# Optimization experiments

Measured on AMD Instinct MI355X. Metric: run time of the kernel, lower is better.

The kernel has to match this reference:

```python
import jax, jax.numpy as jnp
import numpy as np
import math

B, S, H, NH, DK, K = 256, 200, 768, 12, 64, 64
EPS = 1e-12

def setup_inputs() -> dict:
    key = jax.random.key(0)
    ks = jax.random.split(key, 8)
    sc = 0.02
    return {
        "x": jax.random.normal(ks[0], (B, S, H), dtype=jnp.float32),
        "mask": jnp.ones((B, 1, S), dtype=jnp.float32),
        "Wq": jax.random.normal(ks[1], (H, H), dtype=jnp.float32) * sc,
        "bq": jnp.zeros((H,), dtype=jnp.float32),
        "Wk": jax.random.normal(ks[2], (H, H), dtype=jnp.float32) * sc,
        "bk": jnp.zeros((H,), dtype=jnp.float32),
        "Wv": jax.random.normal(ks[3], (H, H), dtype=jnp.float32) * sc,
        "bv": jnp.zeros((H,), dtype=jnp.float32),
        "We": jax.random.normal(ks[4], (K, S), dtype=jnp.float32) * sc,
        "be": jnp.zeros((K,), dtype=jnp.float32),
        "Wf": jax.random.normal(ks[5], (K, S), dtype=jnp.float32) * sc,
        "bf": jnp.zeros((K,), dtype=jnp.float32),
        "Wd": jax.random.normal(ks[6], (H, H), dtype=jnp.float32) * sc,
        "bd": jnp.zeros((H,), dtype=jnp.float32),
        "gamma": jnp.ones((H,), dtype=jnp.float32),
        "beta": jnp.zeros((H,), dtype=jnp.float32),
    }

def _heads(t):  # [B,S,H] -> [B,NH,S,DK]
    return t.reshape(B, S, NH, DK).transpose(0, 2, 1, 3)

def reference(x, mask, Wq, bq, Wk, bk, Wv, bv, We, be, Wf, bf, Wd, bd, gamma, beta):
    q = _heads(x @ Wq.T + bq)
    k = _heads(x @ Wk.T + bk)
    v = _heads(x @ Wv.T + bv)
    m = mask[:, 0:1, :, None]            # [B,1,S,1]
    k = k * m
    v = v * m
    # Linformer seq projections: E on value, F on key (applied along seq axis)
    v = jnp.einsum("bhsd,ks->bhkd", v, We) + be[:, None]   # [B,NH,K,DK]
    k = jnp.einsum("bhsd,ks->bhkd", k, Wf) + bf[:, None]   # [B,NH,K,DK]
    scores = jnp.einsum("bhqd,bhkd->bhqk", q, k) / math.sqrt(DK)
    p_attn = jax.nn.softmax(scores, axis=-1)               # [B,NH,S,K]
    ctx = jnp.einsum("bhqk,bhkd->bhqd", p_attn, v)         # [B,NH,S,DK]
    ctx = ctx.transpose(0, 2, 1, 3).reshape(B, S, H)
    h = ctx @ Wd.T + bd + x                                # dense + residual (dropout=0)
    mu = jnp.mean(h, axis=-1, keepdims=True)
    var = jnp.mean(jnp.square(h - mu), axis=-1, keepdims=True)
    out = (h - mu) / jnp.sqrt(var + EPS) * gamma + beta
    return out, p_attn
```

## Files before the change

### kernel.cpp

```cpp
#include <hip/hip_runtime.h>
#include <stdint.h>

typedef unsigned short u16;
typedef short bf16x8 __attribute__((ext_vector_type(8)));
typedef float f32x4 __attribute__((ext_vector_type(4)));
typedef unsigned short u16x4 __attribute__((ext_vector_type(4)));

#define NB   256
#define NS   200
#define NHID 768
#define NHEAD 12
#define NDK  64
#define NK   64
#define NBH  (NB*NHEAD)
#define NM   (NB*NS)
#define SP   224

__device__ __forceinline__ u16 f2b(float f){
  unsigned u = __builtin_bit_cast(unsigned, f);
  return (u16)((u + 0x7FFFu + ((u>>16)&1u)) >> 16);
}
__device__ __forceinline__ float b2f(u16 b){
  return __builtin_bit_cast(float, (unsigned)b << 16);
}
__device__ __forceinline__ f32x4 mfma16(bf16x8 a, bf16x8 b, f32x4 c){
  return __builtin_amdgcn_mfma_f32_16x16x32_bf16(a, b, c, 0, 0, 0);
}
__device__ __forceinline__ void gload16(u16* l, const u16* g){
  __builtin_amdgcn_global_load_lds(
      (const __attribute__((address_space(1))) void*)g,
      (__attribute__((address_space(3))) void*)l, 16, 0, 0);
}

__global__ __launch_bounds__(256) void prep_kernel(
    const float* __restrict__ Wq, const float* __restrict__ Wk,
    const float* __restrict__ Wv, const float* __restrict__ Wd,
    const float* __restrict__ Wf, const float* __restrict__ We,
    const float* __restrict__ mask,
    u16* __restrict__ Wqb, u16* __restrict__ Wkb,
    u16* __restrict__ Wvb, u16* __restrict__ Wdb,
    u16* __restrict__ Wfeb, float* __restrict__ rs)
{
  const int blk = blockIdx.x, t = threadIdx.x;
  const int i = blk*256 + t;
  Wqb[i]=f2b(Wq[i]); Wkb[i]=f2b(Wk[i]); Wvb[i]=f2b(Wv[i]); Wdb[i]=f2b(Wd[i]);
  if (blk < 128 && t < SP){
    float v = 0.f;
    if (t < NS) v = (blk<64) ? Wf[blk*NS+t] : We[(blk-64)*NS+t];
    Wfeb[blk*SP+t] = f2b(v);
  }
  if (blk >= 1024 && blk < 1280 && t < 128){
    const int b = blk-1024;
    const float* src = (t<64) ? (Wf + t*NS) : (We + (t-64)*NS);
    float acc = 0.f;
    for (int s=0;s<NS;s++) acc += src[s]*mask[b*NS+s];
    rs[b*128+t] = acc;
  }
}

__global__ __launch_bounds__(256) void transpose_x(
    const float* __restrict__ x, const float* __restrict__ mask,
    u16* __restrict__ xb, u16* __restrict__ xbT)
{
  __shared__ u16 LT[64*232];
  const int t = threadIdx.x, b = blockIdx.x, n0 = blockIdx.y*64;
  for (int i=0;i<50;i++){
    const int idx = i*256 + t;
    const int s = idx>>6, n = idx&63;
    const size_t gi = ((size_t)b*NS + s)*NHID + n0 + n;
    const float v = x[gi];
    xb[gi] = f2b(v);
    const float mv = mask[b*NS+s];
    LT[n*232 + s] = f2b(v*mv);
  }
  __syncthreads();
  const int row = t>>2, cb = t&3;
  u16* dst = xbT + (size_t)b*NHID*SP + (size_t)(n0+row)*SP;
  for (int i=0;i<7;i++){
    const int c = cb + i*4;
    bf16x8 vv = (c<25) ? *(const bf16x8*)&LT[row*232 + c*8] : (bf16x8)0;
    *(bf16x8*)&dst[c*8] = vv;
  }
}

__global__ __launch_bounds__(256) void gemm_yfe(
    const u16* __restrict__ Wfeb, const u16* __restrict__ xbT, u16* __restrict__ yfe)
{
  __shared__ u16 Al[128*64];
  __shared__ u16 Bl[128*64];
  const int t=threadIdx.x, w=t>>6, lane=t&63, hi=lane>>4, lo=lane&15;
  const int sr=lane>>3, sc=lane&7;
  const int b=blockIdx.x, col0=blockIdx.y*128;
  const u16* Bg = xbT + (size_t)b*NHID*SP;
  f32x4 acc[4][4];
#pragma unroll
  for(int i=0;i<4;i++)
#pragma unroll
    for(int j=0;j<4;j++) acc[i][j]=(f32x4)0.0f;
  const u16* Ab=&Al[((w>>1)*64+lo)*64 + hi*8];
  const u16* Bb=&Bl[((w&1)*64+lo)*64 + hi*8];

  for (int kt=0; kt<192; kt+=64){
#pragma unroll
    for (int i8=0;i8<4;i8++){
      const int r = w*32 + i8*8 + sr;
      gload16(&Al[r*64 + sc*8], Wfeb + (size_t)r*SP + kt + sc*8);
      gload16(&Bl[r*64 + sc*8], Bg + (size_t)(col0+r)*SP + kt + sc*8);
    }
    asm volatile("s_waitcnt vmcnt(0)" ::: "memory");
    __syncthreads();
#pragma unroll
    for (int ks=0; ks<2; ks++){
      bf16x8 a[4], bfr[4];
#pragma unroll
      for (int i=0;i<4;i++) a[i]   = *(const bf16x8*)(Ab + i*16*64 + ks*32);
#pragma unroll
      for (int j=0;j<4;j++) bfr[j] = *(const bf16x8*)(Bb + j*16*64 + ks*32);
#pragma unroll
      for (int i=0;i<4;i++)
#pragma unroll
        for (int j=0;j<4;j++) acc[i][j] = mfma16(a[i], bfr[j], acc[i][j]);
    }
    __syncthreads();
  }
#pragma unroll
  for (int i8=0;i8<2;i8++){
    const int r2 = w*32 + i8*16 + (lane>>2);
    gload16(&Al[r2*32 + (lane&3)*8], Wfeb + (size_t)r2*SP + 192 + (lane&3)*8);
    gload16(&Bl[r2*32 + (lane&3)*8], Bg + (size_t)(col0+r2)*SP + 192 + (lane&3)*8);
  }
  asm volatile("s_waitcnt vmcnt(0)" ::: "memory");
  __syncthreads();
  {
    bf16x8 a[4], bfr[4];
#pragma unroll
    for (int i=0;i<4;i++) a[i]   = *(const bf16x8*)&Al[((w>>1)*64+i*16+lo)*32 + hi*8];
#pragma unroll
    for (int j=0;j<4;j++) bfr[j] = *(const bf16x8*)&Bl[((w&1)*64+j*16+lo)*32 + hi*8];
#pragma unroll
    for (int i=0;i<4;i++)
#pragma unroll
      for (int j=0;j<4;j++) acc[i][j] = mfma16(a[i], bfr[j], acc[i][j]);
  }
  const int mbase=(w>>1)*64, nbase=col0+(w&1)*64;
#pragma unroll
  for (int i=0;i<4;i++)
#pragma unroll
    for (int r=0;r<4;r++){
      const int m = mbase + i*16 + hi*4 + r;
#pragma unroll
      for (int j=0;j<4;j++){
        const int n = nbase + j*16 + lo;
        yfe[(size_t)b*98304 + (size_t)m*NHID + n] = f2b(acc[i][j][r]);
      }
    }
}

template<int EPI>
__global__ __launch_bounds__(512, 2) void gemm_ring(
    const u16* __restrict__ Ag_, const u16* __restrict__ Bg_,
    const float* __restrict__ bias, const u16* __restrict__ resid,
    u16* __restrict__ Cout)
{
  __shared__ u16 AS[4][8192];
  __shared__ u16 BS[4][8192];
  const int t = threadIdx.x;
  const int w = t>>6, lane = t&63, hi = lane>>4, lo = lane&15;
  const int wm = w>>2, wn = w&3;
  const int bid = blockIdx.x;
  const int row0 = ((bid/24)*8 + (bid&7))*256;
  const int col0 = ((bid>>3)%3)*256;
  const u16* Ag = Ag_ + (size_t)row0*NHID;
  const u16* Bg = Bg_ + (size_t)col0*NHID;
  const int rp0 = t>>3, cc = t&7;

  f32x4 acc[8][4];
#pragma unroll
  for (int i=0;i<8;i++)
#pragma unroll
    for (int j=0;j<4;j++) acc[i][j] = (f32x4)0.0f;

  int aoff[8], boff[4];
#pragma unroll
  for (int i=0;i<8;i++){
    const int r = wm*128 + i*16 + lo;
    const int rp = r>>1, c = (r&1)*4 + hi;
    aoff[i] = rp*64 + ((c ^ (rp&7))<<3);
  }
#pragma unroll
  for (int j=0;j<4;j++){
    const int n = wn*64 + j*16 + lo;
    const int rp = n>>1, c = (n&1)*4 + hi;
    boff[j] = rp*64 + ((c ^ (rp&7))<<3);
  }

  auto stage = [&](int s, int kt){
#pragma unroll
    for (int i8=0;i8<2;i8++){
      const int rp = i8*64 + rp0;
      const int c  = cc ^ (rp&7);
      const int grow = rp*2 + (c>>2);
      const int gcol = (c&3)<<3;
      gload16(&AS[s][rp*64 + cc*8], Ag + (size_t)grow*NHID + kt + gcol);
      gload16(&BS[s][rp*64 + cc*8], Bg + (size_t)grow*NHID + kt + gcol);
    }
  };
  auto body = [&](const u16* as_, const u16* bs_){
    bf16x8 av[8], bvv[4];
#pragma unroll
    for (int j=0;j<4;j++) bvv[j] = *(const bf16x8*)(bs_ + boff[j]);
#pragma unroll
    for (int i=0;i<8;i++) av[i] = *(const bf16x8*)(as_ + aoff[i]);
    __builtin_amdgcn_s_setprio(1);
#pragma unroll
    for (int i=0;i<8;i++)
#pragma unroll
      for (int j=0;j<4;j++) acc[i][j] = mfma16(av[i], bvv[j], acc[i][j]);
    __builtin_amdgcn_s_setprio(0);
  };
  auto step = [&](int tt, int s){
    if (tt+3 < 24) stage((s+3)&3, (tt+3)*32);
    body(AS[s], BS[s]);
    if (tt <= 20)      { asm volatile("s_waitcnt vmcnt(8)" ::: "memory"); }
    else if (tt == 21) { asm volatile("s_waitcnt vmcnt(4)" ::: "memory"); }
    else if (tt == 22) { asm volatile("s_waitcnt vmcnt(0)" ::: "memory"); }
    if (tt < 23){
      __builtin_amdgcn_sched_barrier(0);
      asm volatile("s_barrier" ::: "memory");
      __builtin_amdgcn_sched_barrier(0);
    }
  };

  stage(0,0); stage(1,32); stage(2,64);
  asm volatile("s_waitcnt vmcnt(8)" ::: "memory");
  asm volatile("s_barrier" ::: "memory");
  __builtin_amdgcn_sched_barrier(0);

#pragma unroll
  for (int tt=0; tt<24; tt+=4){
    step(tt,0); step(tt+1,1); step(tt+2,2); step(tt+3,3);
  }

#pragma unroll
  for (int i=0;i<8;i++)
#pragma unroll
    for (int q=0;q<4;q++){
      const int m = row0 + wm*128 + i*16 + hi*4 + q;
#pragma unroll
      for (int j=0;j<4;j++){
        const int n = col0 + wn*64 + j*16 + lo;
        float v = acc[i][j][q] + bias[n];
        if constexpr (EPI==0){
          const int b = m/NS, s = m - b*NS;
          Cout[(((size_t)b*NHEAD + (n>>6))*NS + s)*NDK + (n&63)] = f2b(v);
        } else {
          const size_t gi = (size_t)m*NHID + n;
          Cout[gi] = f2b(v + b2f(resid[gi]));
        }
      }
    }
}

__global__ __launch_bounds__(256) void gemm_projkv(
    const u16* __restrict__ yfe, const u16* __restrict__ Wkb,
    const u16* __restrict__ Wvb, const float* __restrict__ rs,
    const float* __restrict__ bk, const float* __restrict__ bv,
    const float* __restrict__ bff, const float* __restrict__ bee,
    u16* __restrict__ kproj, u16* __restrict__ vout)
{
  __shared__ u16 S[192*64];
  const int t=threadIdx.x, w=t>>6, lane=t&63, hi=lane>>4, lo=lane&15;
  const int sr=lane>>3, sc=lane&7;
  const int bid=blockIdx.x;
  const int b = (bid/96)*8 + (bid&7);
  const int jj = (bid>>3)%12;
  const int colb = jj%6, z = jj/6;

  if (z==0){
    u16* Al = S;
    u16* Bl = S + 64*64;
    const int col0=colb*128;
    const u16* yf = yfe + (size_t)b*98304;
    f32x4 acc[2][4];
#pragma unroll
    for(int i=0;i<2;i++)
#pragma unroll
      for(int j=0;j<4;j++) acc[i][j]=(f32x4)0.0f;
    const u16* Ab=&Al[((w>>1)*32+lo)*64 + hi*8];
    const u16* Bb=&Bl[((w&1)*64+lo)*64 + hi*8];
    for (int kt=0; kt<NHID; kt+=64){
#pragma unroll
      for (int i8=0;i8<2;i8++){
        const int r = w*16 + i8*8 + sr;
        gload16(&Al[r*64 + sc*8], yf + (size_t)r*NHID + kt + sc*8);
      }
#pragma unroll
      for (int i8=0;i8<4;i8++){
        const int r = w*32 + i8*8 + sr;
        gload16(&Bl[r*64 + sc*8], Wkb + (size_t)(col0+r)*NHID + kt + sc*8);
      }
      asm volatile("s_waitcnt vmcnt(0)" ::: "memory");
      __syncthreads();
#pragma unroll
      for (int ks=0; ks<2; ks++){
        bf16x8 a[2], bfr[4];
#pragma unroll
        for (int i=0;i<2;i++) a[i]   = *(const bf16x8*)(Ab + i*16*64 + ks*32);
#pragma unroll
        for (int j=0;j<4;j++) bfr[j] = *(const bf16x8*)(Bb + j*16*64 + ks*32);
#pragma unroll
        for (int i=0;i<2;i++)
#pragma unroll
          for (int j=0;j<4;j++) acc[i][j] = mfma16(a[i], bfr[j], acc[i][j]);
      }
      __syncthreads();
    }
    const int mbase=(w>>1)*32, nbase=col0+(w&1)*64;
#pragma unroll
    for (int i=0;i<2;i++)
#pragma unroll
      for (int r=0;r<4;r++){
        const int m = mbase + i*16 + hi*4 + r;
        const float rsv = rs[b*128 + m], bfv = bff[m];
#pragma unroll
        for (int j=0;j<4;j++){
          const int n = nbase + j*16 + lo;
          kproj[(size_t)b*49152 + (size_t)m*NHID + n] = f2b(acc[i][j][r] + rsv*bk[n] + bfv);
        }
      }
  } else {
    u16* Al = S;
    u16* Bl = S + 128*64;
    const int row0=colb*128;
    const u16* ye = yfe + (size_t)b*98304 + 49152;
    f32x4 acc[4][2];
#pragma unroll
    for(int i=0;i<4;i++)
#pragma unroll
      for(int j=0;j<2;j++) acc[i][j]=(f32x4)0.0f;
    const u16* Ab=&Al[((w>>1)*64+lo)*64 + hi*8];
    const u16* Bb=&Bl[((w&1)*32+lo)*64 + hi*8];
    for (int kt=0; kt<NHID; kt+=64){
#pragma unroll
      for (int i8=0;i8<4;i8++){
        const int r = w*32 + i8*8 + sr;
        gload16(&Al[r*64 + sc*8], Wvb + (size_t)(row0+r)*NHID + kt + sc*8);
      }
#pragma unroll
      for (int i8=0;i8<2;i8++){
        const int r = w*16 + i8*8 + sr;
        gload16(&Bl[r*64 + sc*8], ye + (size_t)r*NHID + kt + sc*8);
      }
      asm volatile("s_waitcnt vmcnt(0)" ::: "memory");
      __syncthreads();
#pragma unroll
      for (int ks=0; ks<2; ks++){
        bf16x8 a[4], bfr[2];
#pragma unroll
        for (int i=0;i<4;i++) a[i]   = *(const bf16x8*)(Ab + i*16*64 + ks*32);
#pragma unroll
        for (int j=0;j<2;j++) bfr[j] = *(const bf16x8*)(Bb + j*16*64 + ks*32);
#pragma unroll
        for (int i=0;i<4;i++)
#pragma unroll
          for (int j=0;j<2;j++) acc[i][j] = mfma16(a[i], bfr[j], acc[i][j]);
      }
      __syncthreads();
    }
    const int mbase=row0+(w>>1)*64, nbase=(w&1)*32;
#pragma unroll
    for (int i=0;i<4;i++)
#pragma unroll
      for (int r=0;r<4;r++){
        const int m = mbase + i*16 + hi*4 + r;
        const float bvv = bv[m];
#pragma unroll
        for (int j=0;j<2;j++){
          const int n = nbase + j*16 + lo;
          vout[(size_t)b*49152 + (size_t)m*64 + n] = f2b(acc[i][j][r] + rs[b*128+64+n]*bvv + bee[n]);
        }
      }
  }
}

__global__ __launch_bounds__(256) void attn_kernel(
    const u16* __restrict__ qb,
    const u16* __restrict__ kproj,
    const u16* __restrict__ vprojT,
    float* __restrict__ pout,
    u16* __restrict__ ctxb)
{
  __shared__ u16 QL[208*72];
  __shared__ u16 KP[64*72];
  __shared__ u16 VP[64*72];
  const int t=threadIdx.x, w=t>>6, lane=t&63, hi=lane>>4, lo=lane&15;
  const int bh = blockIdx.x, b=bh/NHEAD, hh=bh%NHEAD;
  for (int c=t;c<1600;c+=256){
    const int row=c>>3, col8=(c&7)*8;
    *(bf16x8*)&QL[row*72+col8] = *(const bf16x8*)(qb + (size_t)bh*12800 + c*8);
  }
  if (t<72){ const int row=200+t/9, col8=(t%9)*8; *(bf16x8*)&QL[row*72+col8]=(bf16x8)0; }
  for (int c=t;c<512;c+=256){
    const int row=c>>3, col8=(c&7)*8;
    *(bf16x8*)&KP[row*72+col8] = *(const bf16x8*)(kproj  + (size_t)b*49152 + (size_t)row*NHID + hh*64 + col8);
    *(bf16x8*)&VP[row*72+col8] = *(const bf16x8*)(vprojT + (size_t)b*49152 + (size_t)(hh*64+row)*64 + col8);
  }
  __syncthreads();
  const int mf0 = (w==0)?0:(1+w*3);
  const int nmf = (w==0)?4:3;
  f32x4 acc[4][4];
#pragma unroll
  for(int i=0;i<4;i++)
#pragma unroll
    for(int j=0;j<4;j++) acc[i][j]=(f32x4)0.0f;
#pragma unroll
  for (int ks=0; ks<2; ks++){
    bf16x8 a[4], bb[4];
#pragma unroll
    for (int j=0;j<4;j++) bb[j]=*(const bf16x8*)&KP[(j*16+lo)*72 + ks*32 + hi*8];
#pragma unroll
    for (int i=0;i<4;i++) if (i<nmf) a[i]=*(const bf16x8*)&QL[((mf0+i)*16+lo)*72 + ks*32 + hi*8];
#pragma unroll
    for (int i=0;i<4;i++) if (i<nmf)
#pragma unroll
      for (int j=0;j<4;j++)
        acc[i][j]=mfma16(a[i],bb[j],acc[i][j]);
  }
  __syncthreads();

#pragma unroll
  for (int i=0;i<4;i++) if (i<nmf){
#pragma unroll
    for (int r=0;r<4;r++){
      const int q = (mf0+i)*16 + hi*4 + r;
      float s0=acc[i][0][r]*0.125f, s1=acc[i][1][r]*0.125f,
            s2=acc[i][2][r]*0.125f, s3=acc[i][3][r]*0.125f;
      float mx=fmaxf(fmaxf(s0,s1),fmaxf(s2,s3));
      mx=fmaxf(mx,__shfl_xor(mx,1)); mx=fmaxf(mx,__shfl_xor(mx,2));
      mx=fmaxf(mx,__shfl_xor(mx,4)); mx=fmaxf(mx,__shfl_xor(mx,8));
      float e0=__expf(s0-mx), e1=__expf(s1-mx), e2=__expf(s2-mx), e3=__expf(s3-mx);
      float sm=e0+e1+e2+e3;
      sm+=__shfl_xor(sm,1); sm+=__shfl_xor(sm,2); sm+=__shfl_xor(sm,4); sm+=__shfl_xor(sm,8);
      const float inv=1.0f/sm;
      const float p0=e0*inv,p1=e1*inv,p2=e2*inv,p3=e3*inv;
      if (q<NS){
        float* pg = pout + ((size_t)bh*NS + q)*NK + lo;
        pg[0]=p0; pg[16]=p1; pg[32]=p2; pg[48]=p3;
      }
      u16* pl = &QL[q*72 + lo];
      pl[0]=f2b(p0); pl[16]=f2b(p1); pl[32]=f2b(p2); pl[48]=f2b(p3);
    }
  }
  f32x4 acc2[4][4];
#pragma unroll
  for(int i=0;i<4;i++)
#pragma unroll
    for(int j=0;j<4;j++) acc2[i][j]=(f32x4)0.0f;
#pragma unroll
  for (int ks=0; ks<2; ks++){
    bf16x8 a[4], bb[4];
#pragma unroll
    for (int j=0;j<4;j++) bb[j]=*(const bf16x8*)&VP[(j*16+lo)*72 + ks*32 + hi*8];
#pragma unroll
    for (int i=0;i<4;i++) if (i<nmf) a[i]=*(const bf16x8*)&QL[((mf0+i)*16+lo)*72 + ks*32 + hi*8];
#pragma unroll
    for (int i=0;i<4;i++) if (i<nmf)
#pragma unroll
      for (int j=0;j<4;j++)
        acc2[i][j]=mfma16(a[i],bb[j],acc2[i][j]);
  }
#pragma unroll
  for (int i=0;i<4;i++) if (i<nmf)
#pragma unroll
    for (int r=0;r<4;r++){
      const int q=(mf0+i)*16+hi*4+r;
      if (q<NS){
#pragma unroll
        for (int j=0;j<4;j++){
          const int d=j*16+lo;
          ctxb[((size_t)b*NS+q)*NHID + hh*NDK + d] = f2b(acc2[i][j][r]);
        }
      }
    }
}

__global__ __launch_bounds__(256) void ln2_kernel(
    const u16* __restrict__ h, const float* __restrict__ gamma,
    const float* __restrict__ beta, float* __restrict__ outp)
{
  const int t = threadIdx.x, wid = t>>6, lane = t&63;
  float g_[12], be_[12];
#pragma unroll
  for (int k=0;k<3;k++){
    float4 gg = *(const float4*)(gamma + lane*12 + k*4);
    float4 bb = *(const float4*)(beta  + lane*12 + k*4);
    g_[k*4+0]=gg.x; g_[k*4+1]=gg.y; g_[k*4+2]=gg.z; g_[k*4+3]=gg.w;
    be_[k*4+0]=bb.x; be_[k*4+1]=bb.y; be_[k*4+2]=bb.z; be_[k*4+3]=bb.w;
  }
  for (int row = blockIdx.x*4 + wid; row < NM; row += 1600*4){
    const u16* hr = h + (size_t)row*NHID + lane*12;
    u16x4 a0 = *(const u16x4*)hr;
    u16x4 a1 = *(const u16x4*)(hr+4);
    u16x4 a2 = *(const u16x4*)(hr+8);
    float v[12];
#pragma unroll
    for (int k=0;k<4;k++){
      v[k]   = b2f(a0[k]);
      v[4+k] = b2f(a1[k]);
      v[8+k] = b2f(a2[k]);
    }
    float s=0.f, q=0.f;
#pragma unroll
    for (int k=0;k<12;k++){ s+=v[k]; q+=v[k]*v[k]; }
#pragma unroll
    for (int m=1;m<64;m<<=1){ s+=__shfl_xor(s,m); q+=__shfl_xor(q,m); }
    const float mu = s*(1.0f/768.0f);
    const float rsv = rsqrtf(q*(1.0f/768.0f) - mu*mu + 1e-12f);
    float* orow = outp + (size_t)row*NHID + lane*12;
#pragma unroll
    for (int k=0;k<12;k++) orow[k] = (v[k]-mu)*rsv*g_[k] + be_[k];
  }
}

extern "C" void kernel_launch(void* const* d_in, const int* in_sizes, int n_in,
                              void* d_out, int out_size, void* d_ws, size_t ws_size,
                              hipStream_t stream)
{
  (void)in_sizes; (void)n_in; (void)out_size; (void)ws_size;
  const float* x    = (const float*)d_in[0];
  const float* mask = (const float*)d_in[1];
  const float* Wq   = (const float*)d_in[2];
  const float* bq   = (const float*)d_in[3];
  const float* Wk   = (const float*)d_in[4];
  const float* bk   = (const float*)d_in[5];
  const float* Wv   = (const float*)d_in[6];
  const float* bv   = (const float*)d_in[7];
  const float* We   = (const float*)d_in[8];
  const float* be   = (const float*)d_in[9];
  const float* Wf   = (const float*)d_in[10];
  const float* bf   = (const float*)d_in[11];
  const float* Wd   = (const float*)d_in[12];
  const float* bd   = (const float*)d_in[13];
  const float* gamma= (const float*)d_in[14];
  const float* beta = (const float*)d_in[15];

  float* out  = (float*)d_out;
  float* pout = out + (size_t)NM*NHID;

  char* ws = (char*)d_ws;
  u16* xb    = (u16*)(ws);
  u16* xbT   = (u16*)(ws + 78643200ull);
  u16* qb    = (u16*)(ws + 78643200ull);
  u16* yfe   = (u16*)(ws + 166723584ull);
  u16* kproj = (u16*)(ws + 217055232ull);
  u16* Wqb   = (u16*)(ws + 242221056ull);
  u16* Wkb   = (u16*)(ws + 243400704ull);
  u16* Wvb   = (u16*)(ws + 244580352ull);
  u16* Wdb   = (u16*)(ws + 245760000ull);
  u16* Wfeb  = (u16*)(ws + 246939648ull);
  float* rsb = (float*)(ws + 246996992ull);
  u16* vprojT= (u16*)(ws + 247128064ull);
  u16* ctxb  = (u16*)(ws + 272293888ull);
  u16* hb    = (u16*)(ws + 350937088ull);

  prep_kernel<<<2304,256,0,stream>>>(Wq,Wk,Wv,Wd,Wf,We,mask,Wqb,Wkb,Wvb,Wdb,Wfeb,rsb);
  transpose_x<<<dim3(NB,12),256,0,stream>>>(x,mask,xb,xbT);
  gemm_yfe<<<dim3(NB,6),256,0,stream>>>(Wfeb,xbT,yfe);
  gemm_ring<0><<<600,512,0,stream>>>(xb,Wqb,bq,nullptr,qb);
  gemm_projkv<<<3072,256,0,stream>>>(yfe,Wkb,Wvb,rsb,bk,bv,bf,be,kproj,vprojT);
  attn_kernel<<<NBH,256,0,stream>>>(qb,kproj,vprojT,pout,ctxb);
  gemm_ring<1><<<600,512,0,stream>>>(ctxb,Wdb,bd,xb,hb);
  ln2_kernel<<<1600,256,0,stream>>>(hb,gamma,beta,out);
}
```

Measured before the change: 553.0 us.

## Pipeline projkv GEMM with 4-stage swizzled LDS ring and nontemporal output stores

Replaces the single-buffered 64-wide K loop in gemm_projkv with a 4-stage, 32-wide K ring buffer. Global loads are issued three tiles ahead, with partial vmcnt waits and one barrier per step, so memory latency overlaps the MFMA work. The LDS layout is XOR-swizzled to reduce bank conflicts, and s_setprio raises priority around the MFMA bursts. Separately, the p_attn stores and the layernorm output stores become nontemporal, and the layernorm stores are vectorised, to reduce cache pollution from streaming writes.

```diff
diff --git a/kernel.cpp b/kernel.cpp
--- a/kernel.cpp
+++ b/kernel.cpp
@@ -268,54 +268,87 @@
     const float* __restrict__ bff, const float* __restrict__ bee,
     u16* __restrict__ kproj, u16* __restrict__ vout)
 {
-  __shared__ u16 S[192*64];
+  __shared__ u16 S[4][192*32];
   const int t=threadIdx.x, w=t>>6, lane=t&63, hi=lane>>4, lo=lane&15;
-  const int sr=lane>>3, sc=lane&7;
   const int bid=blockIdx.x;
   const int b = (bid/96)*8 + (bid&7);
   const int jj = (bid>>3)%12;
   const int colb = jj%6, z = jj/6;
+  const int cc = t&7, rpt = t>>3;
+
+  const u16* yf  = yfe + (size_t)b*98304;
+  const u16* ye  = yfe + (size_t)b*98304 + 49152;
+  const u16* Wk0 = Wkb + (size_t)(colb*128)*NHID;
+  const u16* Wv0 = Wvb + (size_t)(colb*128)*NHID;
+
+  const u16* srcb[3]; int dsto[3];
+#pragma unroll
+  for (int i8=0;i8<3;i8++){
+    const int rp = i8*32 + rpt;
+    const int c  = cc ^ (rp&7);
+    const int grow = rp*2 + (c>>2);
+    const int gcol = (c&3)<<3;
+    dsto[i8] = rp*64 + cc*8;
+    const u16* rb;
+    if (z==0) rb = (grow<64)  ? (yf  + (size_t)grow*NHID)        : (Wk0 + (size_t)(grow-64)*NHID);
+    else      rb = (grow<128) ? (Wv0 + (size_t)grow*NHID)        : (ye  + (size_t)(grow-128)*NHID);
+    srcb[i8] = rb + gcol;
+  }
+  auto off = [&](int r){
+    const int rp = r>>1, c = (r&1)*4 + hi;
+    return rp*64 + ((c ^ (rp&7))<<3);
+  };
+  auto stage = [&](int s, int kt){
+#pragma unroll
+    for (int i8=0;i8<3;i8++) gload16(&S[s][dsto[i8]], srcb[i8] + kt);
+  };
 
   if (z==0){
-    u16* Al = S;
-    u16* Bl = S + 64*64;
-    const int col0=colb*128;
-    const u16* yf = yfe + (size_t)b*98304;
+    int aoff[2], boff[4];
+#pragma unroll
+    for (int i=0;i<2;i++) aoff[i] = off((w>>1)*32 + i*16 + lo);
+#pragma unroll
+    for (int j=0;j<4;j++) boff[j] = off(64 + (w&1)*64 + j*16 + lo);
     f32x4 acc[2][4];
 #pragma unroll
     for(int i=0;i<2;i++)
 #pragma unroll
       for(int j=0;j<4;j++) acc[i][j]=(f32x4)0.0f;
-    const u16* Ab=&Al[((w>>1)*32+lo)*64 + hi*8];
-    const u16* Bb=&Bl[((w&1)*64+lo)*64 + hi*8];
-    for (int kt=0; kt<NHID; kt+=64){
-#pragma unroll
-      for (int i8=0;i8<2;i8++){
-        const int r = w*16 + i8*8 + sr;
-        gload16(&Al[r*64 + sc*8], yf + (size_t)r*NHID + kt + sc*8);
-      }
-#pragma unroll
-      for (int i8=0;i8<4;i8++){
-        const int r = w*32 + i8*8 + sr;
-        gload16(&Bl[r*64 + sc*8], Wkb + (size_t)(col0+r)*NHID + kt + sc*8);
-      }
-      asm volatile("s_waitcnt vmcnt(0)" ::: "memory");
-      __syncthreads();
-#pragma unroll
-      for (int ks=0; ks<2; ks++){
-        bf16x8 a[2], bfr[4];
-#pragma unroll
-        for (int i=0;i<2;i++) a[i]   = *(const bf16x8*)(Ab + i*16*64 + ks*32);
-#pragma unroll
-        for (int j=0;j<4;j++) bfr[j] = *(const bf16x8*)(Bb + j*16*64 + ks*32);
-#pragma unroll
-        for (int i=0;i<2;i++)
-#pragma unroll
-          for (int j=0;j<4;j++) acc[i][j] = mfma16(a[i], bfr[j], acc[i][j]);
-      }
-      __syncthreads();
-    }
-    const int mbase=(w>>1)*32, nbase=col0+(w&1)*64;
+
+    auto body = [&](const u16* ss){
+      bf16x8 af[2], bfr[4];
+#pragma unroll
+      for (int j=0;j<4;j++) bfr[j] = *(const bf16x8*)(ss + boff[j]);
+#pragma unroll
+      for (int i=0;i<2;i++) af[i]  = *(const bf16x8*)(ss + aoff[i]);
+      __builtin_amdgcn_s_setprio(1);
+#pragma unroll
+      for (int i=0;i<2;i++)
+#pragma unroll
+        for (int j=0;j<4;j++) acc[i][j] = mfma16(af[i], bfr[j], acc[i][j]);
+      __builtin_amdgcn_s_setprio(0);
+    };
+    auto step = [&](int tt, int s){
+      if (tt+3 < 24) stage((s+3)&3, (tt+3)*32);
+      body(S[s]);
+      if (tt <= 20)      { asm volatile("s_waitcnt vmcnt(6)" ::: "memory"); }
+      else if (tt == 21) { asm volatile("s_waitcnt vmcnt(3)" ::: "memory"); }
+      else if (tt == 22) { asm volatile("s_waitcnt vmcnt(0)" ::: "memory"); }
+      if (tt < 23){
+        __builtin_amdgcn_sched_barrier(0);
+        asm volatile("s_barrier" ::: "memory");
+        __builtin_amdgcn_sched_barrier(0);
+      }
+    };
+    stage(0,0); stage(1,32); stage(2,64);
+    asm volatile("s_waitcnt vmcnt(6)" ::: "memory");
+    asm volatile("s_barrier" ::: "memory");
+    __builtin_amdgcn_sched_barrier(0);
+#pragma unroll
+    for (int tt=0; tt<24; tt+=4){
+      step(tt,0); step(tt+1,1); step(tt+2,2); step(tt+3,3);
+    }
+    const int mbase=(w>>1)*32, nbase=colb*128+(w&1)*64;
 #pragma unroll
     for (int i=0;i<2;i++)
 #pragma unroll
@@ -329,45 +362,51 @@
         }
       }
   } else {
-    u16* Al = S;
-    u16* Bl = S + 128*64;
-    const int row0=colb*128;
-    const u16* ye = yfe + (size_t)b*98304 + 49152;
+    int aoff[4], boff[2];
+#pragma unroll
+    for (int i=0;i<4;i++) aoff[i] = off((w>>1)*64 + i*16 + lo);
+#pragma unroll
+    for (int j=0;j<2;j++) boff[j] = off(128 + (w&1)*32 + j*16 + lo);
     f32x4 acc[4][2];
 #pragma unroll
     for(int i=0;i<4;i++)
 #pragma unroll
       for(int j=0;j<2;j++) acc[i][j]=(f32x4)0.0f;
-    const u16* Ab=&Al[((w>>1)*64+lo)*64 + hi*8];
-    const u16* Bb=&Bl[((w&1)*32+lo)*64 + hi*8];
-    for (int kt=0; kt<NHID; kt+=64){
-#pragma unroll
-      for (int i8=0;i8<4;i8++){
-        const int r = w*32 + i8*8 + sr;
-        gload16(&Al[r*64 + sc*8], Wvb + (size_t)(row0+r)*NHID + kt + sc*8);
-      }
-#pragma unroll
-      for (int i8=0;i8<2;i8++){
-        const int r = w*16 + i8*8 + sr;
-        gload16(&Bl[r*64 + sc*8], ye + (size_t)r*NHID + kt + sc*8);
-      }
-      asm volatile("s_waitcnt vmcnt(0)" ::: "memory");
-      __syncthreads();
-#pragma unroll
-      for (int ks=0; ks<2; ks++){
-        bf16x8 a[4], bfr[2];
-#pragma unroll
-        for (int i=0;i<4;i++) a[i]   = *(const bf16x8*)(Ab + i*16*64 + ks*32);
-#pragma unroll
-        for (int j=0;j<2;j++) bfr[j] = *(const bf16x8*)(Bb + j*16*64 + ks*32);
-#pragma unroll
-        for (int i=0;i<4;i++)
-#pragma unroll
-          for (int j=0;j<2;j++) acc[i][j] = mfma16(a[i], bfr[j], acc[i][j]);
-      }
-      __syncthreads();
-    }
-    const int mbase=row0+(w>>1)*64, nbase=(w&1)*32;
+
+    auto body = [&](const u16* ss){
+      bf16x8 af[4], bfr[2];
+#pragma unroll
+      for (int j=0;j<2;j++) bfr[j] = *(const bf16x8*)(ss + boff[j]);
+#pragma unroll
+      for (int i=0;i<4;i++) af[i]  = *(const bf16x8*)(ss + aoff[i]);
+      __builtin_amdgcn_s_setprio(1);
+#pragma unroll
+      for (int i=0;i<4;i++)
+#pragma unroll
+        for (int j=0;j<2;j++) acc[i][j] = mfma16(af[i], bfr[j], acc[i][j]);
+      __builtin_amdgcn_s_setprio(0);
+    };
+    auto step = [&](int tt, int s){
+      if (tt+3 < 24) stage((s+3)&3, (tt+3)*32);
+      body(S[s]);
+      if (tt <= 20)      { asm volatile("s_waitcnt vmcnt(6)" ::: "memory"); }
+      else if (tt == 21) { asm volatile("s_waitcnt vmcnt(3)" ::: "memory"); }
+      else if (tt == 22) { asm volatile("s_waitcnt vmcnt(0)" ::: "memory"); }
+      if (tt < 23){
+        __builtin_amdgcn_sched_barrier(0);
+        asm volatile("s_barrier" ::: "memory");
+        __builtin_amdgcn_sched_barrier(0);
+      }
+    };
+    stage(0,0); stage(1,32); stage(2,64);
+    asm volatile("s_waitcnt vmcnt(6)" ::: "memory");
+    asm volatile("s_barrier" ::: "memory");
+    __builtin_amdgcn_sched_barrier(0);
+#pragma unroll
+    for (int tt=0; tt<24; tt+=4){
+      step(tt,0); step(tt+1,1); step(tt+2,2); step(tt+3,3);
+    }
+    const int mbase=colb*128+(w>>1)*64, nbase=(w&1)*32;
 #pragma unroll
     for (int i=0;i<4;i++)
 #pragma unroll
@@ -445,7 +484,10 @@
       const float p0=e0*inv,p1=e1*inv,p2=e2*inv,p3=e3*inv;
       if (q<NS){
         float* pg = pout + ((size_t)bh*NS + q)*NK + lo;
-        pg[0]=p0; pg[16]=p1; pg[32]=p2; pg[48]=p3;
+        __builtin_nontemporal_store(p0, pg);
+        __builtin_nontemporal_store(p1, pg+16);
+        __builtin_nontemporal_store(p2, pg+32);
+        __builtin_nontemporal_store(p3, pg+48);
       }
       u16* pl = &QL[q*72 + lo];
       pl[0]=f2b(p0); pl[16]=f2b(p1); pl[32]=f2b(p2); pl[48]=f2b(p3);
@@ -518,7 +560,14 @@
     const float rsv = rsqrtf(q*(1.0f/768.0f) - mu*mu + 1e-12f);
     float* orow = outp + (size_t)row*NHID + lane*12;
 #pragma unroll
-    for (int k=0;k<12;k++) orow[k] = (v[k]-mu)*rsv*g_[k] + be_[k];
+    for (int k=0;k<3;k++){
+      f32x4 o;
+      o[0]=(v[k*4+0]-mu)*rsv*g_[k*4+0]+be_[k*4+0];
+      o[1]=(v[k*4+1]-mu)*rsv*g_[k*4+1]+be_[k*4+1];
+      o[2]=(v[k*4+2]-mu)*rsv*g_[k*4+2]+be_[k*4+2];
+      o[3]=(v[k*4+3]-mu)*rsv*g_[k*4+3]+be_[k*4+3];
+      __builtin_nontemporal_store(o, (f32x4*)&orow[k*4]);
+    }
   }
 }
 
```

Result: slower. 575.1 us (+4.0%).

## Fuse masked x transpose into seq-projection GEMM and vectorize x conversion

Applied to the files above, without the earlier changes.

Removes the intermediate transposed, masked bf16 copy of x (xbT). The sequence-projection GEMM now reads fp32 x directly, applies the mask, converts to bf16 and writes it transposed into swizzled LDS. A separate vectorized kernel converts x to bf16 for the Q GEMM. This drops a large intermediate write and read, at the cost of the yfe GEMM doing register-staged conversion in place of async global-to-LDS loads, plus an extra K tile padded to 256.

```diff
diff --git a/kernel.cpp b/kernel.cpp
--- a/kernel.cpp
+++ b/kernel.cpp
@@ -14,7 +14,6 @@
 #define NK   64
 #define NBH  (NB*NHEAD)
 #define NM   (NB*NS)
-#define SP   224
 
 __device__ __forceinline__ u16 f2b(float f){
   unsigned u = __builtin_bit_cast(unsigned, f);
@@ -22,6 +21,12 @@
 }
 __device__ __forceinline__ float b2f(u16 b){
   return __builtin_bit_cast(float, (unsigned)b << 16);
+}
+__device__ __forceinline__ bf16x8 pack8(const float* v){
+  bf16x8 r;
+#pragma unroll
+  for (int i=0;i<8;i++) r[i] = (short)f2b(v[i]);
+  return r;
 }
 __device__ __forceinline__ f32x4 mfma16(bf16x8 a, bf16x8 b, f32x4 c){
   return __builtin_amdgcn_mfma_f32_16x16x32_bf16(a, b, c, 0, 0, 0);
@@ -44,10 +49,10 @@
   const int blk = blockIdx.x, t = threadIdx.x;
   const int i = blk*256 + t;
   Wqb[i]=f2b(Wq[i]); Wkb[i]=f2b(Wk[i]); Wvb[i]=f2b(Wv[i]); Wdb[i]=f2b(Wd[i]);
-  if (blk < 128 && t < SP){
+  if (blk < 128){
     float v = 0.f;
     if (t < NS) v = (blk<64) ? Wf[blk*NS+t] : We[(blk-64)*NS+t];
-    Wfeb[blk*SP+t] = f2b(v);
+    Wfeb[blk*256+t] = f2b(v);
   }
   if (blk >= 1024 && blk < 1280 && t < 128){
     const int b = blk-1024;
@@ -58,54 +63,71 @@
   }
 }
 
-__global__ __launch_bounds__(256) void transpose_x(
+__global__ __launch_bounds__(256) void convert_x(
+    const float* __restrict__ x, u16* __restrict__ xb)
+{
+  const size_t i = ((size_t)blockIdx.x*256 + threadIdx.x)*8;
+  float4 a0 = *(const float4*)(x+i), a1 = *(const float4*)(x+i+4);
+  float ta[8] = {a0.x,a0.y,a0.z,a0.w,a1.x,a1.y,a1.z,a1.w};
+  *(bf16x8*)(xb+i) = pack8(ta);
+}
+
+__global__ __launch_bounds__(256) void gemm_yfe2(
     const float* __restrict__ x, const float* __restrict__ mask,
-    u16* __restrict__ xb, u16* __restrict__ xbT)
-{
-  __shared__ u16 LT[64*232];
-  const int t = threadIdx.x, b = blockIdx.x, n0 = blockIdx.y*64;
-  for (int i=0;i<50;i++){
-    const int idx = i*256 + t;
-    const int s = idx>>6, n = idx&63;
-    const size_t gi = ((size_t)b*NS + s)*NHID + n0 + n;
-    const float v = x[gi];
-    xb[gi] = f2b(v);
-    const float mv = mask[b*NS+s];
-    LT[n*232 + s] = f2b(v*mv);
-  }
-  __syncthreads();
-  const int row = t>>2, cb = t&3;
-  u16* dst = xbT + (size_t)b*NHID*SP + (size_t)(n0+row)*SP;
-  for (int i=0;i<7;i++){
-    const int c = cb + i*4;
-    bf16x8 vv = (c<25) ? *(const bf16x8*)&LT[row*232 + c*8] : (bf16x8)0;
-    *(bf16x8*)&dst[c*8] = vv;
-  }
-}
-
-__global__ __launch_bounds__(256) void gemm_yfe(
-    const u16* __restrict__ Wfeb, const u16* __restrict__ xbT, u16* __restrict__ yfe)
+    const u16* __restrict__ Wfeb, u16* __restrict__ yfe)
 {
   __shared__ u16 Al[128*64];
-  __shared__ u16 Bl[128*64];
+  __shared__ u16 Bl[128*72];
+  __shared__ float Ml[256];
   const int t=threadIdx.x, w=t>>6, lane=t&63, hi=lane>>4, lo=lane&15;
   const int sr=lane>>3, sc=lane&7;
   const int b=blockIdx.x, col0=blockIdx.y*128;
-  const u16* Bg = xbT + (size_t)b*NHID*SP;
+  const int a16 = t&15, q4 = t>>4;
+  const int ss0 = q4*4;
+  const int swzw = (a16&7)<<3;
+
+  Ml[t] = (t<NS) ? mask[b*NS+t] : 0.f;
+
   f32x4 acc[4][4];
 #pragma unroll
   for(int i=0;i<4;i++)
 #pragma unroll
     for(int j=0;j<4;j++) acc[i][j]=(f32x4)0.0f;
+
   const u16* Ab=&Al[((w>>1)*64+lo)*64 + hi*8];
-  const u16* Bb=&Bl[((w&1)*64+lo)*64 + hi*8];
-
-  for (int kt=0; kt<192; kt+=64){
+  int nb_[4], sw_[4];
+#pragma unroll
+  for (int j=0;j<4;j++){
+    const int n = (w&1)*64 + j*16 + lo;
+    nb_[j] = n*72;
+    sw_[j] = ((n>>3)&7)<<3;
+  }
+  __syncthreads();
+
+  for (int kt=0; kt<256; kt+=64){
 #pragma unroll
     for (int i8=0;i8<4;i8++){
       const int r = w*32 + i8*8 + sr;
-      gload16(&Al[r*64 + sc*8], Wfeb + (size_t)r*SP + kt + sc*8);
-      gload16(&Bl[r*64 + sc*8], Bg + (size_t)(col0+r)*SP + kt + sc*8);
+      gload16(&Al[r*64 + sc*8], Wfeb + (size_t)r*256 + kt + sc*8);
+    }
+    float vv[4][8];
+#pragma unroll
+    for (int ii=0;ii<4;ii++){
+      const int s = kt + ss0 + ii;
+      const int srow = (s<NS) ? s : (NS-1);
+      const float* gp = x + ((size_t)b*NS + srow)*NHID + col0 + a16*8;
+      float4 u0 = *(const float4*)gp, u1 = *(const float4*)(gp+4);
+      const float m = Ml[s];
+      vv[ii][0]=u0.x*m; vv[ii][1]=u0.y*m; vv[ii][2]=u0.z*m; vv[ii][3]=u0.w*m;
+      vv[ii][4]=u1.x*m; vv[ii][5]=u1.y*m; vv[ii][6]=u1.z*m; vv[ii][7]=u1.w*m;
+    }
+    const int ss_swz = ss0 ^ swzw;
+#pragma unroll
+    for (int h=0;h<8;h++){
+      u16x4 p;
+      p[0]=f2b(vv[0][h]); p[1]=f2b(vv[1][h]);
+      p[2]=f2b(vv[2][h]); p[3]=f2b(vv[3][h]);
+      *(u16x4*)&Bl[(a16*8+h)*72 + ss_swz] = p;
     }
     asm volatile("s_waitcnt vmcnt(0)" ::: "memory");
     __syncthreads();
@@ -115,32 +137,16 @@
 #pragma unroll
       for (int i=0;i<4;i++) a[i]   = *(const bf16x8*)(Ab + i*16*64 + ks*32);
 #pragma unroll
-      for (int j=0;j<4;j++) bfr[j] = *(const bf16x8*)(Bb + j*16*64 + ks*32);
+      for (int j=0;j<4;j++){
+        const int s8 = ks*32 + hi*8;
+        bfr[j] = *(const bf16x8*)&Bl[nb_[j] + (s8 ^ sw_[j])];
+      }
 #pragma unroll
       for (int i=0;i<4;i++)
 #pragma unroll
         for (int j=0;j<4;j++) acc[i][j] = mfma16(a[i], bfr[j], acc[i][j]);
     }
     __syncthreads();
-  }
-#pragma unroll
-  for (int i8=0;i8<2;i8++){
-    const int r2 = w*32 + i8*16 + (lane>>2);
-    gload16(&Al[r2*32 + (lane&3)*8], Wfeb + (size_t)r2*SP + 192 + (lane&3)*8);
-    gload16(&Bl[r2*32 + (lane&3)*8], Bg + (size_t)(col0+r2)*SP + 192 + (lane&3)*8);
-  }
-  asm volatile("s_waitcnt vmcnt(0)" ::: "memory");
-  __syncthreads();
-  {
-    bf16x8 a[4], bfr[4];
-#pragma unroll
-    for (int i=0;i<4;i++) a[i]   = *(const bf16x8*)&Al[((w>>1)*64+i*16+lo)*32 + hi*8];
-#pragma unroll
-    for (int j=0;j<4;j++) bfr[j] = *(const bf16x8*)&Bl[((w&1)*64+j*16+lo)*32 + hi*8];
-#pragma unroll
-    for (int i=0;i<4;i++)
-#pragma unroll
-      for (int j=0;j<4;j++) acc[i][j] = mfma16(a[i], bfr[j], acc[i][j]);
   }
   const int mbase=(w>>1)*64, nbase=col0+(w&1)*64;
 #pragma unroll
@@ -549,7 +555,6 @@
 
   char* ws = (char*)d_ws;
   u16* xb    = (u16*)(ws);
-  u16* xbT   = (u16*)(ws + 78643200ull);
   u16* qb    = (u16*)(ws + 78643200ull);
   u16* yfe   = (u16*)(ws + 166723584ull);
   u16* kproj = (u16*)(ws + 217055232ull);
@@ -558,14 +563,14 @@
   u16* Wvb   = (u16*)(ws + 244580352ull);
   u16* Wdb   = (u16*)(ws + 245760000ull);
   u16* Wfeb  = (u16*)(ws + 246939648ull);
-  float* rsb = (float*)(ws + 246996992ull);
-  u16* vprojT= (u16*)(ws + 247128064ull);
-  u16* ctxb  = (u16*)(ws + 272293888ull);
-  u16* hb    = (u16*)(ws + 350937088ull);
+  float* rsb = (float*)(ws + 247005184ull);
+  u16* vprojT= (u16*)(ws + 247136256ull);
+  u16* ctxb  = (u16*)(ws + 272302080ull);
+  u16* hb    = (u16*)(ws + 350945280ull);
 
   prep_kernel<<<2304,256,0,stream>>>(Wq,Wk,Wv,Wd,Wf,We,mask,Wqb,Wkb,Wvb,Wdb,Wfeb,rsb);
-  transpose_x<<<dim3(NB,12),256,0,stream>>>(x,mask,xb,xbT);
-  gemm_yfe<<<dim3(NB,6),256,0,stream>>>(Wfeb,xbT,yfe);
+  convert_x<<<19200,256,0,stream>>>(x,xb);
+  gemm_yfe2<<<dim3(NB,6),256,0,stream>>>(x,mask,Wfeb,yfe);
   gemm_ring<0><<<600,512,0,stream>>>(xb,Wqb,bq,nullptr,qb);
   gemm_projkv<<<3072,256,0,stream>>>(yfe,Wkb,Wvb,rsb,bk,bv,bf,be,kproj,vprojT);
   attn_kernel<<<NBH,256,0,stream>>>(qb,kproj,vprojT,pout,ctxb);
```

After: 533.2 us. -3.6%, faster.
